# Kernel tuning notes

Measured on AMD Instinct MI355X. Metric: run time of the kernel, lower is better.

Reference implementation:

```python
import jax, jax.numpy as jnp
import numpy as np

N_NODES = 100_000
N_EDGES = 1_600_000
N_GRAPHS = 100
NODES_PER_GRAPH = N_NODES // N_GRAPHS
C_IN = 64
C_EDGE = 16
HIDDEN = 64
N_LAYERS = 3
MLP_HIDDEN = 256
N_CLASSES = 4
ENC = 16  # encoding_size; marker column = ENC-1
BN_EPS = 1e-5


def setup_inputs() -> dict:
    key = jax.random.key(0)
    ks = jax.random.split(key, 12)
    spec_idx = jnp.arange(N_GRAPHS, dtype=jnp.int32) * NODES_PER_GRAPH
    x = jax.random.normal(ks[0], (N_NODES, C_IN), jnp.float32)
    # exactly one specified node per graph: x[:, ENC-1] == 1 only at spec_idx
    x = x.at[:, ENC - 1].set(0.0)
    x = x.at[spec_idx, ENC - 1].set(1.0)
    # edges confined within each graph
    eg = jax.random.randint(ks[1], (N_EDGES,), 0, N_GRAPHS)
    src = eg * NODES_PER_GRAPH + jax.random.randint(ks[2], (N_EDGES,), 0, NODES_PER_GRAPH)
    dst = eg * NODES_PER_GRAPH + jax.random.randint(ks[3], (N_EDGES,), 0, NODES_PER_GRAPH)
    edge_index = jnp.stack([src, dst]).astype(jnp.int32)
    edge_attr = jax.random.normal(ks[4], (N_EDGES, C_EDGE), jnp.float32)
    batch = jnp.repeat(jnp.arange(N_GRAPHS, dtype=jnp.int32), NODES_PER_GRAPH)
    neighbor = jax.random.normal(ks[5], (N_GRAPHS, C_IN), jnp.float32)
    msg_in = 2 * HIDDEN + C_EDGE  # 144 (C_IN == HIDDEN)
    s = 1.0 / np.sqrt(msg_in)
    W = jax.random.normal(ks[6], (N_LAYERS, msg_in, HIDDEN), jnp.float32) * s
    b = jax.random.normal(ks[7], (N_LAYERS, HIDDEN), jnp.float32) * s
    bn_gamma = jnp.ones((N_LAYERS, HIDDEN), jnp.float32)
    bn_beta = jnp.zeros((N_LAYERS, HIDDEN), jnp.float32)
    fc1_in = HIDDEN + C_IN + N_LAYERS * HIDDEN  # 320
    fc1_w = jax.random.normal(ks[8], (fc1_in, MLP_HIDDEN), jnp.float32) / np.sqrt(fc1_in)
    fc1_b = jax.random.normal(ks[9], (MLP_HIDDEN,), jnp.float32) / np.sqrt(fc1_in)
    fc2_w = jax.random.normal(ks[10], (MLP_HIDDEN, N_CLASSES), jnp.float32) / np.sqrt(MLP_HIDDEN)
    fc2_b = jax.random.normal(ks[11], (N_CLASSES,), jnp.float32) / np.sqrt(MLP_HIDDEN)
    return {"x": x, "edge_attr": edge_attr, "neighbor": neighbor, "W": W, "b": b,
            "bn_gamma": bn_gamma, "bn_beta": bn_beta, "fc1_w": fc1_w, "fc1_b": fc1_b,
            "fc2_w": fc2_w, "fc2_b": fc2_b, "edge_index": edge_index, "batch": batch,
            "spec_idx": spec_idx}


def reference(x, edge_attr, neighbor, W, b, bn_gamma, bn_beta,
              fc1_w, fc1_b, fc2_w, fc2_b, edge_index, batch, spec_idx):
    N = x.shape[0]
    loops = jnp.arange(N, dtype=edge_index.dtype)
    src = jnp.concatenate([edge_index[0], loops])   # x_j (source)
    dst = jnp.concatenate([edge_index[1], loops])   # x_i (target / aggregate)
    ea = jnp.concatenate([edge_attr, jnp.ones((N, edge_attr.shape[1]), x.dtype)], axis=0)
    bn_scale = 1.0 / jnp.sqrt(jnp.float32(1.0) + BN_EPS)  # eval BN: mean=0, var=1
    embs = []
    for l in range(W.shape[0]):
        # gather -> linear on concat(x_i, x_j, e) -> scatter-add
        m = jnp.concatenate([x[dst], x[src], ea], axis=1) @ W[l] + b[l]  # [E+N, H]
        agg = jax.ops.segment_sum(m, dst, num_segments=N)                # [N, H]
        h = jax.nn.relu(agg)                       # relu inside MP layer
        h = bn_gamma[l] * h * bn_scale + bn_beta[l]  # BatchNorm1d (eval)
        x = jax.nn.relu(h)                         # relu after BN (dropout=eval no-op)
        embs.append(x[spec_idx])
    B = spec_idx.shape[0]
    pooled = jax.ops.segment_sum(x, batch, num_segments=B)  # global_add_pool [B, H]
    feats = jnp.concatenate([pooled] + embs + [neighbor], axis=1)  # [B, 320]
    h = jax.nn.relu(feats @ fc1_w + fc1_b)
    return h @ fc2_w + fc2_b
```

## Files before the change

kernel.cpp:

```cpp
#include <hip/hip_runtime.h>
#include <hip/hip_bf16.h>

#define NN 100000
#define NE 1600000
#define NG 100
#define NPG 1000
#define CE 16
#define HH 64
#define BN_SCALE 0.99999500003749959f
#define NB 512
#define ECH (NE / NB)
#define NBIN 400
#define NRANGE 12500


typedef __attribute__((ext_vector_type(8))) short bf16x8;
typedef __attribute__((ext_vector_type(4))) float f32x4;
union ABu { bf16x8 f; ushort u[8]; };

__device__ __forceinline__ ushort f2bf_rne(float f) {
  unsigned u = __float_as_uint(f);
  return (ushort)((u + 0x7FFFu + ((u >> 16) & 1u)) >> 16);
}

__global__ __launch_bounds__(256) void k_hist(const int* __restrict__ ei,
                                              int* __restrict__ hist) {
  __shared__ int h[NBIN];
  for (int i = threadIdx.x; i < NBIN; i += 256) h[i] = 0;
  __syncthreads();
  int e0 = blockIdx.x * ECH;
  for (int i = threadIdx.x; i < ECH; i += 256) {
    int d = ei[NE + e0 + i];
    atomicAdd(&h[d / 250], 1);
  }
  __syncthreads();
  for (int i = threadIdx.x; i < NBIN; i += 256) hist[blockIdx.x * NBIN + i] = h[i];
}

__global__ __launch_bounds__(512) void k_scan_a(const int* __restrict__ hist,
                                                int* __restrict__ partial,
                                                int* __restrict__ gtot) {
  __shared__ int sv[512];
  int bin = blockIdx.x, t = threadIdx.x;
  int v = (t < NB) ? hist[t * NBIN + bin] : 0;
  sv[t] = v;
  __syncthreads();
  for (int o = 1; o < 512; o <<= 1) {
    int a = (t >= o) ? sv[t - o] : 0;
    __syncthreads();
    sv[t] += a;
    __syncthreads();
  }
  if (t < NB) partial[t * NBIN + bin] = sv[t] - v;
  if (t == 511) gtot[bin] = sv[511];
}

__global__ __launch_bounds__(512) void k_scan_b(const int* __restrict__ gtot,
                                                int* __restrict__ gbase) {
  __shared__ int sv[512];
  int t = threadIdx.x;
  int v = (t < NBIN) ? gtot[t] : 0;
  sv[t] = v;
  __syncthreads();
  for (int o = 1; o < 512; o <<= 1) {
    int a = (t >= o) ? sv[t - o] : 0;
    __syncthreads();
    sv[t] += a;
    __syncthreads();
  }
  if (t < NBIN) gbase[t] = sv[t] - v;
  if (t == 511) gbase[NBIN] = sv[511];
}

__global__ __launch_bounds__(256) void k_bfill(const int* __restrict__ ei,
                                               const int* __restrict__ partial,
                                               const int* __restrict__ gbase,
                                               unsigned long long* __restrict__ ebuf) {
  __shared__ int cur[NBIN];
  int b = blockIdx.x;
  for (int i = threadIdx.x; i < NBIN; i += 256)
    cur[i] = gbase[i] + partial[b * NBIN + i];
  __syncthreads();
  int e0 = b * ECH;
  for (int i = threadIdx.x; i < ECH; i += 256) {
    int e = e0 + i;
    int d = ei[NE + e], s = ei[e];
    int bin = d / 250;
    int gb = (bin >> 2) * 1000;
    unsigned long long pk = (unsigned long long)(unsigned)e << 32 |
                            (unsigned)((d - gb) << 10) | (unsigned)(s - gb);
    int pos = atomicAdd(&cur[bin], 1);
    ebuf[pos] = pk;
  }
}

__global__ __launch_bounds__(1024) void k_nsort(
    const unsigned long long* __restrict__ ebuf, const int* __restrict__ gbase,
    unsigned* __restrict__ ebuf2, int* __restrict__ rowptr,
    int* __restrict__ cnt) {
  __shared__ int h[250];
  __shared__ int cur[250];
  __shared__ int sv[256];
  int bin = blockIdx.x, t = threadIdx.x;
  int nb = bin * 250, lbase = (bin & 3) * 250;
  int lo = gbase[bin], hi = gbase[bin + 1];
  if (t < 250) h[t] = 0;
  __syncthreads();
  for (int i = lo + t; i < hi; i += 1024) {
    int dl = (int)((ebuf[i] >> 10) & 1023);
    atomicAdd(&h[dl - lbase], 1);
  }
  __syncthreads();
  int v = (t < 250) ? h[t] : 0;
  if (t < 256) sv[t] = v;
  __syncthreads();
  for (int o = 1; o < 256; o <<= 1) {
    int a = (t < 256 && t >= o) ? sv[t - o] : 0;
    __syncthreads();
    if (t < 256) sv[t] += a;
    __syncthreads();
  }
  if (t < 250) {
    int base = lo + sv[t] - v;
    rowptr[nb + t] = base;
    cur[t] = base;
    cnt[nb + t] = v;
  }
  if (bin == NBIN - 1 && t == 0) rowptr[NN] = hi;
  __syncthreads();
  for (int i = lo + t; i < hi; i += 1024) {
    unsigned long long u = ebuf[i];
    int dl = (int)((u >> 10) & 1023);
    unsigned pk = (unsigned)(u >> 32) << 10 | (unsigned)(u & 1023);
    int pos = atomicAdd(&cur[dl - lbase], 1);
    ebuf2[pos] = pk;
  }
}

#define SEB 25000
__global__ __launch_bounds__(256) void k_se3(const unsigned* __restrict__ ebuf2,
                                             const int* __restrict__ rowptr,
                                             const float* __restrict__ ea,
                                             ushort* __restrict__ Se16) {
  int lane = threadIdx.x & 63;
  int slot = lane >> 2;
  int q = lane & 3;
  int orig = blockIdx.x;
  int blk = (orig & 7) * (SEB / 8) + (orig >> 3);
  int n0 = blk * 4 + (threadIdx.x >> 6);
  if (n0 >= NN) return;
  int n = __builtin_amdgcn_readfirstlane(n0);
  int lo = rowptr[n], hi = rowptr[n + 1];
  float aA0 = 0.f, aA1 = 0.f, aA2 = 0.f, aA3 = 0.f;
  float aB0 = 0.f, aB1 = 0.f, aB2 = 0.f, aB3 = 0.f;
  for (int k0 = lo; k0 < hi; k0 += 32) {
    int ka = k0 + slot, kb = k0 + 16 + slot;
    int kca = min(ka, NE - 1), kcb = min(kb, NE - 1);
    unsigned eida = ebuf2[kca] >> 10;
    unsigned eidb = ebuf2[kcb] >> 10;
    float4 va = *(const float4*)(ea + (size_t)eida * CE + q * 4);
    float4 vb = *(const float4*)(ea + (size_t)eidb * CE + q * 4);
    bool oka = ka < hi, okb = kb < hi;
    aA0 += oka ? va.x : 0.f;
    aA1 += oka ? va.y : 0.f;
    aA2 += oka ? va.z : 0.f;
    aA3 += oka ? va.w : 0.f;
    aB0 += okb ? vb.x : 0.f;
    aB1 += okb ? vb.y : 0.f;
    aB2 += okb ? vb.z : 0.f;
    aB3 += okb ? vb.w : 0.f;
  }
  float r0 = aA0 + aB0, r1 = aA1 + aB1, r2 = aA2 + aB2, r3 = aA3 + aB3;
#pragma unroll
  for (int o = 4; o < 64; o <<= 1) {
    r0 += __shfl_xor(r0, o);
    r1 += __shfl_xor(r1, o);
    r2 += __shfl_xor(r2, o);
    r3 += __shfl_xor(r3, o);
  }
  if (lane < 4) {
    unsigned lo32 = (unsigned)f2bf_rne(r0) | ((unsigned)f2bf_rne(r1) << 16);
    unsigned hi32 = (unsigned)f2bf_rne(r2) | ((unsigned)f2bf_rne(r3) << 16);
    *(uint2*)(Se16 + (size_t)n * 16 + lane * 4) = make_uint2(lo32, hi32);
  }
}

__global__ __launch_bounds__(256) void k_cvt(const float* __restrict__ xin,
                                             ushort* __restrict__ xb) {
  int i = blockIdx.x * 256 + threadIdx.x;
  float4 v = ((const float4*)xin)[i];
  ushort4 o;
  o.x = f2bf_rne(v.x); o.y = f2bf_rne(v.y);
  o.z = f2bf_rne(v.z); o.w = f2bf_rne(v.w);
  ((ushort4*)xb)[i] = o;
}

#define GEMM_TILES (NN / 16)
#define GB 512
__global__ __attribute__((amdgpu_waves_per_eu(2, 4))) __launch_bounds__(256)
void k_gemm(const ushort* __restrict__ x, const float* __restrict__ W,
            const float* __restrict__ b, const int* __restrict__ cnt,
            const ushort* __restrict__ Se16, ushort* __restrict__ y,
            ushort* __restrict__ z) {
  int lane = threadIdx.x & 63;
  int g = lane >> 4, r16 = lane & 15;

  ABu Bm[8][2];
  ABu Bs[4];
  float bias4[4];
#pragma unroll
  for (int t = 0; t < 8; ++t) {
    int col = t * 16 + r16;
    const float* wbase = W + (col < 64 ? 0 : 64 * 64);
    int c64 = col & 63;
#pragma unroll
    for (int h = 0; h < 2; ++h)
#pragma unroll
      for (int e = 0; e < 8; ++e) {
        int k = h * 32 + (e < 4 ? 0 : 16) + 4 * g + (e & 3);
        Bm[t][h].u[e] = f2bf_rne(wbase[k * 64 + c64]);
      }
  }
#pragma unroll
  for (int t = 0; t < 4; ++t) {
    int col = t * 16 + r16;
    float ws = 0.f;
#pragma unroll
    for (int m = 0; m < 16; ++m) ws += W[(128 + m) * 64 + col];
#pragma unroll
    for (int e = 0; e < 8; ++e) {
      int k = (e < 4 ? 0 : 16) + 4 * g + (e & 3);
      float v = (k < 16) ? W[(128 + k) * 64 + col] : (k == 16 ? ws : 0.f);
      Bs[t].u[e] = f2bf_rne(v);
    }
    bias4[t] = b[col];
  }

  int wid = (blockIdx.x << 2) + (threadIdx.x >> 6);
  int nw = GB * 4;
  for (int tt = wid; tt < GEMM_TILES; tt += nw) {
    int nb = tt * 16;
    const ushort* xr = x + (size_t)(nb + r16) * 64;
    ABu A0, A1, AS;
    *(ushort4*)&A0.u[0] = *(const ushort4*)(xr + 4 * g);
    *(ushort4*)&A0.u[4] = *(const ushort4*)(xr + 16 + 4 * g);
    *(ushort4*)&A1.u[0] = *(const ushort4*)(xr + 32 + 4 * g);
    *(ushort4*)&A1.u[4] = *(const ushort4*)(xr + 48 + 4 * g);
    const ushort* sr = Se16 + (size_t)(nb + r16) * 16;
    *(ushort4*)&AS.u[0] = *(const ushort4*)(sr + 4 * g);
    AS.u[4] = (g == 0) ? (ushort)0x3F80 : (ushort)0;
    AS.u[5] = 0; AS.u[6] = 0; AS.u[7] = 0;
    float dq[4];
#pragma unroll
    for (int q = 0; q < 4; ++q) dq[q] = (float)(cnt[nb + 4 * g + q] + 1);

    f32x4 accM[8], accS[4];
#pragma unroll
    for (int t = 0; t < 8; ++t) {
      f32x4 zz = {0.f, 0.f, 0.f, 0.f};
      zz = __builtin_amdgcn_mfma_f32_16x16x32_bf16(A0.f, Bm[t][0].f, zz, 0, 0, 0);
      accM[t] = __builtin_amdgcn_mfma_f32_16x16x32_bf16(A1.f, Bm[t][1].f, zz, 0, 0, 0);
    }
#pragma unroll
    for (int t = 0; t < 4; ++t) {
      f32x4 zz = {0.f, 0.f, 0.f, 0.f};
      accS[t] = __builtin_amdgcn_mfma_f32_16x16x32_bf16(AS.f, Bs[t].f, zz, 0, 0, 0);
    }
#pragma unroll
    for (int q = 0; q < 4; ++q) {
      size_t node = (size_t)(nb + 4 * g + q);
      ushort* zp = z + node * 64 + r16;
      ushort* yp = y + node * 64 + r16;
#pragma unroll
      for (int t = 0; t < 4; ++t) {
        float zv = dq[q] * (accM[t][q] + bias4[t]) + accS[t][q];
        zp[t * 16] = f2bf_rne(zv);
        yp[t * 16] = f2bf_rne(accM[4 + t][q]);
      }
    }
  }
}

#define GTB 25000
__global__ __launch_bounds__(256) void k_gath3(
    const __hip_bfloat16* __restrict__ y, const __hip_bfloat16* __restrict__ z,
    const unsigned* __restrict__ ebuf2, const int* __restrict__ rowptr,
    const float* __restrict__ gamma, const float* __restrict__ beta,
    __hip_bfloat16* __restrict__ xn, float* __restrict__ emb) {
  int lane = threadIdx.x & 63;
  int orig = blockIdx.x;
  int blk = (orig & 7) * (GTB / 8) + (orig >> 3);
  int n0 = blk * 4 + (threadIdx.x >> 6);
  if (n0 >= NN) return;
  int n = __builtin_amdgcn_readfirstlane(n0);
  int lo = rowptr[n], hi = rowptr[n + 1];
  int deg = hi - lo;
  int gb = (n / NPG) * NPG;
  const unsigned* cl = ebuf2 + lo;
  const __hip_bfloat16* yg = y + (size_t)gb * HH;
  float acc = __bfloat162float(z[(size_t)n * HH + lane]) +
              __bfloat162float(y[(size_t)n * HH + lane]);
  int k = 0;
  for (; k + 8 <= deg; k += 8) {
    int s0 = cl[k] & 1023, s1 = cl[k + 1] & 1023;
    int s2 = cl[k + 2] & 1023, s3 = cl[k + 3] & 1023;
    int s4 = cl[k + 4] & 1023, s5 = cl[k + 5] & 1023;
    int s6 = cl[k + 6] & 1023, s7 = cl[k + 7] & 1023;
    float v0 = __bfloat162float(yg[(size_t)s0 * HH + lane]);
    float v1 = __bfloat162float(yg[(size_t)s1 * HH + lane]);
    float v2 = __bfloat162float(yg[(size_t)s2 * HH + lane]);
    float v3 = __bfloat162float(yg[(size_t)s3 * HH + lane]);
    float v4 = __bfloat162float(yg[(size_t)s4 * HH + lane]);
    float v5 = __bfloat162float(yg[(size_t)s5 * HH + lane]);
    float v6 = __bfloat162float(yg[(size_t)s6 * HH + lane]);
    float v7 = __bfloat162float(yg[(size_t)s7 * HH + lane]);
    acc += ((v0 + v1) + (v2 + v3)) + ((v4 + v5) + (v6 + v7));
  }
  for (; k < deg; ++k)
    acc += __bfloat162float(yg[(size_t)(cl[k] & 1023) * HH + lane]);
  acc = fmaxf(acc, 0.f);
  acc = gamma[lane] * acc * BN_SCALE + beta[lane];
  acc = fmaxf(acc, 0.f);
  xn[(size_t)n * HH + lane] = __float2bfloat16(acc);
  if (n % NPG == 0) emb[(n / NPG) * HH + lane] = acc;
}

__global__ __launch_bounds__(512) void k_pool(const __hip_bfloat16* __restrict__ xf,
                                              float* __restrict__ partial) {
  __shared__ float pp[8][64];
  int bin = blockIdx.x;
  int lane = threadIdx.x & 63, wv = threadIdx.x >> 6;
  const __hip_bfloat16* base = xf + (size_t)bin * 250 * HH;
  float acc = 0.f;
  int i = wv;
  for (; i + 24 < 250; i += 32) {
    float v0 = __bfloat162float(base[(size_t)i * HH + lane]);
    float v1 = __bfloat162float(base[(size_t)(i + 8) * HH + lane]);
    float v2 = __bfloat162float(base[(size_t)(i + 16) * HH + lane]);
    float v3 = __bfloat162float(base[(size_t)(i + 24) * HH + lane]);
    acc += (v0 + v1) + (v2 + v3);
  }
  for (; i < 250; i += 8) acc += __bfloat162float(base[(size_t)i * HH + lane]);
  pp[wv][lane] = acc;
  __syncthreads();
  if (wv == 0) {
    float s = ((pp[0][lane] + pp[1][lane]) + (pp[2][lane] + pp[3][lane])) +
              ((pp[4][lane] + pp[5][lane]) + (pp[6][lane] + pp[7][lane]));
    partial[bin * 64 + lane] = s;
  }
}

__global__ __launch_bounds__(256) void k_final(
    const float* __restrict__ partial, const float* __restrict__ emb,
    const float* __restrict__ nbr, const float* __restrict__ fc1w,
    const float* __restrict__ fc1b, const float* __restrict__ fc2w,
    const float* __restrict__ fc2b, float* __restrict__ out) {
  __shared__ float feats[320];
  __shared__ float r1[256];
  __shared__ float red[4][4];
  int g = blockIdx.x;
  int t = threadIdx.x;
  if (t < 64) {
    const float* pb = partial + 4 * g * 64;
    feats[t] = (pb[t] + pb[64 + t]) + (pb[128 + t] + pb[192 + t]);
    feats[256 + t] = nbr[(size_t)g * HH + t];
  } else {
    int j = t - 64;
    feats[64 + j] = emb[((size_t)(j >> 6) * NG + g) * HH + (j & 63)];
  }
  __syncthreads();
  float a0 = fc1b[t], a1 = 0.f, a2 = 0.f, a3 = 0.f;
  const float* wp = fc1w + t;
  for (int k = 0; k < 320; k += 8) {
    float w0 = wp[(k + 0) * 256], w1 = wp[(k + 1) * 256];
    float w2 = wp[(k + 2) * 256], w3 = wp[(k + 3) * 256];
    float w4 = wp[(k + 4) * 256], w5 = wp[(k + 5) * 256];
    float w6 = wp[(k + 6) * 256], w7 = wp[(k + 7) * 256];
    a0 = fmaf(feats[k], w0, a0);
    a1 = fmaf(feats[k + 1], w1, a1);
    a2 = fmaf(feats[k + 2], w2, a2);
    a3 = fmaf(feats[k + 3], w3, a3);
    a0 = fmaf(feats[k + 4], w4, a0);
    a1 = fmaf(feats[k + 5], w5, a1);
    a2 = fmaf(feats[k + 6], w6, a2);
    a3 = fmaf(feats[k + 7], w7, a3);
  }
  float rv = fmaxf((a0 + a1) + (a2 + a3), 0.f);
  r1[t] = rv;
  float p0 = rv * fc2w[t * 4 + 0];
  float p1 = rv * fc2w[t * 4 + 1];
  float p2 = rv * fc2w[t * 4 + 2];
  float p3 = rv * fc2w[t * 4 + 3];
#pragma unroll
  for (int o = 1; o < 64; o <<= 1) {
    p0 += __shfl_xor(p0, o);
    p1 += __shfl_xor(p1, o);
    p2 += __shfl_xor(p2, o);
    p3 += __shfl_xor(p3, o);
  }
  if ((t & 63) == 0) {
    int wv = t >> 6;
    red[wv][0] = p0; red[wv][1] = p1; red[wv][2] = p2; red[wv][3] = p3;
  }
  __syncthreads();
  if (t < 4)
    out[g * 4 + t] = fc2b[t] +
                     ((red[0][t] + red[1][t]) + (red[2][t] + red[3][t]));
}

extern "C" void kernel_launch(void* const* d_in, const int* in_sizes, int n_in,
                              void* d_out, int out_size, void* d_ws, size_t ws_size,
                              hipStream_t stream) {
  const float* x     = (const float*)d_in[0];
  const float* eattr = (const float*)d_in[1];
  const float* nbr   = (const float*)d_in[2];
  const float* W     = (const float*)d_in[3];
  const float* b     = (const float*)d_in[4];
  const float* gamma = (const float*)d_in[5];
  const float* beta  = (const float*)d_in[6];
  const float* fc1w  = (const float*)d_in[7];
  const float* fc1b  = (const float*)d_in[8];
  const float* fc2w  = (const float*)d_in[9];
  const float* fc2b  = (const float*)d_in[10];
  const int*   ei    = (const int*)d_in[11];
  float* out = (float*)d_out;
  (void)in_sizes; (void)n_in; (void)out_size; (void)ws_size;

  char* p = (char*)d_ws;
  size_t off = 0;
  auto alloc = [&](size_t bytes) {
    char* q = p + off;
    off += (bytes + 255) & ~(size_t)255;
    return q;
  };
  int* hist    = (int*)alloc((size_t)NB * NBIN * 4);
  int* partial = (int*)alloc((size_t)NB * NBIN * 4);
  int* gtot    = (int*)alloc((size_t)NBIN * 4);
  int* gbase   = (int*)alloc((size_t)(NBIN + 1) * 4);
  unsigned long long* ebuf = (unsigned long long*)alloc((size_t)NE * 8);
  unsigned* ebuf2 = (unsigned*)alloc((size_t)NE * 4);
  int* rowptr  = (int*)alloc((size_t)(NN + 1) * 4);
  ushort* Se16 = (ushort*)alloc((size_t)NN * 16 * 2);
  int*   cnt   = (int*)alloc((size_t)NN * 4);
  ushort* xbf  = (ushort*)alloc((size_t)NN * HH * 2);
  ushort* ybuf = (ushort*)alloc((size_t)NN * HH * 2);
  ushort* zbuf = (ushort*)alloc((size_t)NN * HH * 2);
  ushort* xA   = (ushort*)alloc((size_t)NN * HH * 2);
  ushort* xB   = (ushort*)alloc((size_t)NN * HH * 2);
  float* emb   = (float*)alloc((size_t)3 * NG * HH * 4);
  float* pool  = (float*)alloc((size_t)NBIN * HH * 4);

  k_hist<<<NB, 256, 0, stream>>>(ei, hist);
  k_scan_a<<<NBIN, 512, 0, stream>>>(hist, partial, gtot);
  k_scan_b<<<1, 512, 0, stream>>>(gtot, gbase);
  k_bfill<<<NB, 256, 0, stream>>>(ei, partial, gbase, ebuf);
  k_nsort<<<NBIN, 1024, 0, stream>>>(ebuf, gbase, ebuf2, rowptr, cnt);
  k_se3<<<SEB, 256, 0, stream>>>(ebuf2, rowptr, eattr, Se16);
  k_cvt<<<NN * HH / 4 / 256, 256, 0, stream>>>(x, xbf);

  k_gemm<<<GB, 256, 0, stream>>>(xbf, W, b, cnt, Se16, ybuf, zbuf);
  k_gath3<<<GTB, 256, 0, stream>>>((const __hip_bfloat16*)ybuf,
                                   (const __hip_bfloat16*)zbuf, ebuf2, rowptr,
                                   gamma, beta, (__hip_bfloat16*)xA, emb);
  k_gemm<<<GB, 256, 0, stream>>>(xA, W + 144 * 64, b + 64, cnt, Se16, ybuf, zbuf);
  k_gath3<<<GTB, 256, 0, stream>>>((const __hip_bfloat16*)ybuf,
                                   (const __hip_bfloat16*)zbuf, ebuf2, rowptr,
                                   gamma + 64, beta + 64, (__hip_bfloat16*)xB,
                                   emb + NG * HH);
  k_gemm<<<GB, 256, 0, stream>>>(xB, W + 2 * 144 * 64, b + 128, cnt, Se16, ybuf,
                                 zbuf);
  k_gath3<<<GTB, 256, 0, stream>>>((const __hip_bfloat16*)ybuf,
                                   (const __hip_bfloat16*)zbuf, ebuf2, rowptr,
                                   gamma + 128, beta + 128, (__hip_bfloat16*)xA,
                                   emb + 2 * NG * HH);

  k_pool<<<NBIN, 512, 0, stream>>>((const __hip_bfloat16*)xA, pool);
  k_final<<<NG, 256, 0, stream>>>(pool, emb, nbr, fc1w, fc1b, fc2w, fc2b, out);
}
```

Baseline: 261.3 us.

## Aggregate raw neighbor features before GEMM and fuse BN/ReLU into GEMM epilogue

Reorders each message-passing layer so neighbor features are summed first (gather-then-transform) and the source-side weight is applied to the aggregated sum in the GEMM, instead of transforming every node and then gathering transformed rows. The BN/ReLU epilogue and the spec-node embedding write move into the GEMM, and the first layer reads fp32 x directly, which removes the separate conversion kernel and the y/z intermediate buffers. The gather kernel now processes two nodes per wave with paired loads and clamped, predicated tails. The GEMM gains extra MFMAs and another A operand load per tile. The first-layer gather reads fp32 rows, doubling its traffic for that layer.

```diff
diff --git a/kernel.cpp b/kernel.cpp
--- a/kernel.cpp
+++ b/kernel.cpp
@@ -11,7 +11,6 @@
 #define NB 512
 #define ECH (NE / NB)
 #define NBIN 400
-#define NRANGE 12500
 
 
 typedef __attribute__((ext_vector_type(8))) short bf16x8;
@@ -185,45 +184,93 @@
   }
 }
 
-__global__ __launch_bounds__(256) void k_cvt(const float* __restrict__ xin,
-                                             ushort* __restrict__ xb) {
-  int i = blockIdx.x * 256 + threadIdx.x;
-  float4 v = ((const float4*)xin)[i];
-  ushort4 o;
-  o.x = f2bf_rne(v.x); o.y = f2bf_rne(v.y);
-  o.z = f2bf_rne(v.z); o.w = f2bf_rne(v.w);
-  ((ushort4*)xb)[i] = o;
+#define GXB 12500
+template <typename T>
+__device__ __forceinline__ void ldpair(const T* xg, unsigned srcl, int c,
+                                       float& p0, float& p1) {
+  if constexpr (sizeof(T) == 4) {
+    const float* p = (const float*)xg + (size_t)srcl * HH + 2 * c;
+    p0 = p[0];
+    p1 = p[1];
+  } else {
+    unsigned u = *(const unsigned*)((const ushort*)xg + (size_t)srcl * HH + 2 * c);
+    p0 = __uint_as_float(u << 16);
+    p1 = __uint_as_float(u & 0xffff0000u);
+  }
+}
+
+template <typename T>
+__global__ __launch_bounds__(256) void k_gathx(const T* __restrict__ x,
+                                               const unsigned* __restrict__ ebuf2,
+                                               const int* __restrict__ rowptr,
+                                               ushort* __restrict__ Sx) {
+  int lane = threadIdx.x & 63;
+  int h = lane >> 5, c = lane & 31;
+  int pr = blockIdx.x * 4 + (threadIdx.x >> 6);
+  int n = pr * 2 + h;
+  int lo = rowptr[n], hi = rowptr[n + 1];
+  int deg = hi - lo;
+  int gb = (n / NPG) * NPG;
+  const T* xg = x + (size_t)gb * HH;
+  float a0, a1;
+  ldpair(x, (unsigned)n, c, a0, a1);
+  int kend = hi - 1;
+  for (int k = 0; k < deg; k += 8) {
+    int k0 = lo + k;
+    int c0 = min(k0 + 0, kend), c1 = min(k0 + 1, kend);
+    int c2 = min(k0 + 2, kend), c3 = min(k0 + 3, kend);
+    int c4 = min(k0 + 4, kend), c5 = min(k0 + 5, kend);
+    int c6 = min(k0 + 6, kend), c7 = min(k0 + 7, kend);
+    unsigned s0 = ebuf2[c0] & 1023u, s1 = ebuf2[c1] & 1023u;
+    unsigned s2 = ebuf2[c2] & 1023u, s3 = ebuf2[c3] & 1023u;
+    unsigned s4 = ebuf2[c4] & 1023u, s5 = ebuf2[c5] & 1023u;
+    unsigned s6 = ebuf2[c6] & 1023u, s7 = ebuf2[c7] & 1023u;
+    float v00, v01, v10, v11, v20, v21, v30, v31;
+    float v40, v41, v50, v51, v60, v61, v70, v71;
+    ldpair(xg, s0, c, v00, v01);
+    ldpair(xg, s1, c, v10, v11);
+    ldpair(xg, s2, c, v20, v21);
+    ldpair(xg, s3, c, v30, v31);
+    ldpair(xg, s4, c, v40, v41);
+    ldpair(xg, s5, c, v50, v51);
+    ldpair(xg, s6, c, v60, v61);
+    ldpair(xg, s7, c, v70, v71);
+    bool o0 = k + 0 < deg, o1 = k + 1 < deg, o2 = k + 2 < deg, o3 = k + 3 < deg;
+    bool o4 = k + 4 < deg, o5 = k + 5 < deg, o6 = k + 6 < deg, o7 = k + 7 < deg;
+    a0 += (o0 ? v00 : 0.f) + (o1 ? v10 : 0.f) + (o2 ? v20 : 0.f) + (o3 ? v30 : 0.f);
+    a1 += (o0 ? v01 : 0.f) + (o1 ? v11 : 0.f) + (o2 ? v21 : 0.f) + (o3 ? v31 : 0.f);
+    a0 += (o4 ? v40 : 0.f) + (o5 ? v50 : 0.f) + (o6 ? v60 : 0.f) + (o7 ? v70 : 0.f);
+    a1 += (o4 ? v41 : 0.f) + (o5 ? v51 : 0.f) + (o6 ? v61 : 0.f) + (o7 ? v71 : 0.f);
+  }
+  unsigned w = (unsigned)f2bf_rne(a0) | ((unsigned)f2bf_rne(a1) << 16);
+  *(unsigned*)(Sx + (size_t)n * HH + 2 * c) = w;
 }
 
 #define GEMM_TILES (NN / 16)
 #define GB 512
+template <typename T>
 __global__ __attribute__((amdgpu_waves_per_eu(2, 4))) __launch_bounds__(256)
-void k_gemm(const ushort* __restrict__ x, const float* __restrict__ W,
-            const float* __restrict__ b, const int* __restrict__ cnt,
-            const ushort* __restrict__ Se16, ushort* __restrict__ y,
-            ushort* __restrict__ z) {
+void k_gemm2(const T* __restrict__ x, const ushort* __restrict__ Sx,
+             const float* __restrict__ W, const float* __restrict__ b,
+             const int* __restrict__ cnt, const ushort* __restrict__ Se16,
+             const float* __restrict__ gamma, const float* __restrict__ beta,
+             ushort* __restrict__ xn, float* __restrict__ embL) {
   int lane = threadIdx.x & 63;
   int g = lane >> 4, r16 = lane & 15;
 
-  ABu Bm[8][2];
-  ABu Bs[4];
-  float bias4[4];
-#pragma unroll
-  for (int t = 0; t < 8; ++t) {
-    int col = t * 16 + r16;
-    const float* wbase = W + (col < 64 ? 0 : 64 * 64);
-    int c64 = col & 63;
-#pragma unroll
-    for (int h = 0; h < 2; ++h)
-#pragma unroll
-      for (int e = 0; e < 8; ++e) {
-        int k = h * 32 + (e < 4 ? 0 : 16) + 4 * g + (e & 3);
-        Bm[t][h].u[e] = f2bf_rne(wbase[k * 64 + c64]);
-      }
-  }
+  ABu Bi[4][2], Bj[4][2], Bs[4];
+  float bias4[4], gam4[4], bet4[4];
 #pragma unroll
   for (int t = 0; t < 4; ++t) {
     int col = t * 16 + r16;
+#pragma unroll
+    for (int hh = 0; hh < 2; ++hh)
+#pragma unroll
+      for (int e = 0; e < 8; ++e) {
+        int k = hh * 32 + (e < 4 ? 0 : 16) + 4 * g + (e & 3);
+        Bi[t][hh].u[e] = f2bf_rne(W[k * 64 + col]);
+        Bj[t][hh].u[e] = f2bf_rne(W[(64 + k) * 64 + col]);
+      }
     float ws = 0.f;
 #pragma unroll
     for (int m = 0; m < 16; ++m) ws += W[(128 + m) * 64 + col];
@@ -234,18 +281,41 @@
       Bs[t].u[e] = f2bf_rne(v);
     }
     bias4[t] = b[col];
+    gam4[t] = gamma[col] * BN_SCALE;
+    bet4[t] = beta[col];
   }
 
   int wid = (blockIdx.x << 2) + (threadIdx.x >> 6);
   int nw = GB * 4;
   for (int tt = wid; tt < GEMM_TILES; tt += nw) {
     int nb = tt * 16;
-    const ushort* xr = x + (size_t)(nb + r16) * 64;
-    ABu A0, A1, AS;
-    *(ushort4*)&A0.u[0] = *(const ushort4*)(xr + 4 * g);
-    *(ushort4*)&A0.u[4] = *(const ushort4*)(xr + 16 + 4 * g);
-    *(ushort4*)&A1.u[0] = *(const ushort4*)(xr + 32 + 4 * g);
-    *(ushort4*)&A1.u[4] = *(const ushort4*)(xr + 48 + 4 * g);
+    ABu A0, A1, X0, X1, AS;
+    if constexpr (sizeof(T) == 4) {
+      const float* xr = (const float*)x + (size_t)(nb + r16) * HH;
+      float4 f0 = *(const float4*)(xr + 4 * g);
+      float4 f1 = *(const float4*)(xr + 16 + 4 * g);
+      float4 f2 = *(const float4*)(xr + 32 + 4 * g);
+      float4 f3 = *(const float4*)(xr + 48 + 4 * g);
+      A0.u[0] = f2bf_rne(f0.x); A0.u[1] = f2bf_rne(f0.y);
+      A0.u[2] = f2bf_rne(f0.z); A0.u[3] = f2bf_rne(f0.w);
+      A0.u[4] = f2bf_rne(f1.x); A0.u[5] = f2bf_rne(f1.y);
+      A0.u[6] = f2bf_rne(f1.z); A0.u[7] = f2bf_rne(f1.w);
+      A1.u[0] = f2bf_rne(f2.x); A1.u[1] = f2bf_rne(f2.y);
+      A1.u[2] = f2bf_rne(f2.z); A1.u[3] = f2bf_rne(f2.w);
+      A1.u[4] = f2bf_rne(f3.x); A1.u[5] = f2bf_rne(f3.y);
+      A1.u[6] = f2bf_rne(f3.z); A1.u[7] = f2bf_rne(f3.w);
+    } else {
+      const ushort* xr = (const ushort*)x + (size_t)(nb + r16) * HH;
+      *(ushort4*)&A0.u[0] = *(const ushort4*)(xr + 4 * g);
+      *(ushort4*)&A0.u[4] = *(const ushort4*)(xr + 16 + 4 * g);
+      *(ushort4*)&A1.u[0] = *(const ushort4*)(xr + 32 + 4 * g);
+      *(ushort4*)&A1.u[4] = *(const ushort4*)(xr + 48 + 4 * g);
+    }
+    const ushort* sxr = Sx + (size_t)(nb + r16) * HH;
+    *(ushort4*)&X0.u[0] = *(const ushort4*)(sxr + 4 * g);
+    *(ushort4*)&X0.u[4] = *(const ushort4*)(sxr + 16 + 4 * g);
+    *(ushort4*)&X1.u[0] = *(const ushort4*)(sxr + 32 + 4 * g);
+    *(ushort4*)&X1.u[4] = *(const ushort4*)(sxr + 48 + 4 * g);
     const ushort* sr = Se16 + (size_t)(nb + r16) * 16;
     *(ushort4*)&AS.u[0] = *(const ushort4*)(sr + 4 * g);
     AS.u[4] = (g == 0) ? (ushort)0x3F80 : (ushort)0;
@@ -254,75 +324,33 @@
 #pragma unroll
     for (int q = 0; q < 4; ++q) dq[q] = (float)(cnt[nb + 4 * g + q] + 1);
 
-    f32x4 accM[8], accS[4];
-#pragma unroll
-    for (int t = 0; t < 8; ++t) {
-      f32x4 zz = {0.f, 0.f, 0.f, 0.f};
-      zz = __builtin_amdgcn_mfma_f32_16x16x32_bf16(A0.f, Bm[t][0].f, zz, 0, 0, 0);
-      accM[t] = __builtin_amdgcn_mfma_f32_16x16x32_bf16(A1.f, Bm[t][1].f, zz, 0, 0, 0);
-    }
+    f32x4 accI[4], accR[4];
 #pragma unroll
     for (int t = 0; t < 4; ++t) {
       f32x4 zz = {0.f, 0.f, 0.f, 0.f};
-      accS[t] = __builtin_amdgcn_mfma_f32_16x16x32_bf16(AS.f, Bs[t].f, zz, 0, 0, 0);
+      zz = __builtin_amdgcn_mfma_f32_16x16x32_bf16(A0.f, Bi[t][0].f, zz, 0, 0, 0);
+      accI[t] = __builtin_amdgcn_mfma_f32_16x16x32_bf16(A1.f, Bi[t][1].f, zz, 0, 0, 0);
+      f32x4 rr = {0.f, 0.f, 0.f, 0.f};
+      rr = __builtin_amdgcn_mfma_f32_16x16x32_bf16(X0.f, Bj[t][0].f, rr, 0, 0, 0);
+      rr = __builtin_amdgcn_mfma_f32_16x16x32_bf16(X1.f, Bj[t][1].f, rr, 0, 0, 0);
+      accR[t] = __builtin_amdgcn_mfma_f32_16x16x32_bf16(AS.f, Bs[t].f, rr, 0, 0, 0);
     }
 #pragma unroll
     for (int q = 0; q < 4; ++q) {
-      size_t node = (size_t)(nb + 4 * g + q);
-      ushort* zp = z + node * 64 + r16;
-      ushort* yp = y + node * 64 + r16;
+      int node = nb + 4 * g + q;
+      ushort* xp = xn + (size_t)node * 64 + r16;
+      bool spec = (node % NPG) == 0;
 #pragma unroll
       for (int t = 0; t < 4; ++t) {
-        float zv = dq[q] * (accM[t][q] + bias4[t]) + accS[t][q];
-        zp[t * 16] = f2bf_rne(zv);
-        yp[t * 16] = f2bf_rne(accM[4 + t][q]);
+        float zv = dq[q] * (accI[t][q] + bias4[t]) + accR[t][q];
+        zv = fmaxf(zv, 0.f);
+        zv = gam4[t] * zv + bet4[t];
+        zv = fmaxf(zv, 0.f);
+        xp[t * 16] = f2bf_rne(zv);
+        if (spec) embL[(node / NPG) * HH + t * 16 + r16] = zv;
       }
     }
   }
-}
-
-#define GTB 25000
-__global__ __launch_bounds__(256) void k_gath3(
-    const __hip_bfloat16* __restrict__ y, const __hip_bfloat16* __restrict__ z,
-    const unsigned* __restrict__ ebuf2, const int* __restrict__ rowptr,
-    const float* __restrict__ gamma, const float* __restrict__ beta,
-    __hip_bfloat16* __restrict__ xn, float* __restrict__ emb) {
-  int lane = threadIdx.x & 63;
-  int orig = blockIdx.x;
-  int blk = (orig & 7) * (GTB / 8) + (orig >> 3);
-  int n0 = blk * 4 + (threadIdx.x >> 6);
-  if (n0 >= NN) return;
-  int n = __builtin_amdgcn_readfirstlane(n0);
-  int lo = rowptr[n], hi = rowptr[n + 1];
-  int deg = hi - lo;
-  int gb = (n / NPG) * NPG;
-  const unsigned* cl = ebuf2 + lo;
-  const __hip_bfloat16* yg = y + (size_t)gb * HH;
-  float acc = __bfloat162float(z[(size_t)n * HH + lane]) +
-              __bfloat162float(y[(size_t)n * HH + lane]);
-  int k = 0;
-  for (; k + 8 <= deg; k += 8) {
-    int s0 = cl[k] & 1023, s1 = cl[k + 1] & 1023;
-    int s2 = cl[k + 2] & 1023, s3 = cl[k + 3] & 1023;
-    int s4 = cl[k + 4] & 1023, s5 = cl[k + 5] & 1023;
-    int s6 = cl[k + 6] & 1023, s7 = cl[k + 7] & 1023;
-    float v0 = __bfloat162float(yg[(size_t)s0 * HH + lane]);
-    float v1 = __bfloat162float(yg[(size_t)s1 * HH + lane]);
-    float v2 = __bfloat162float(yg[(size_t)s2 * HH + lane]);
-    float v3 = __bfloat162float(yg[(size_t)s3 * HH + lane]);
-    float v4 = __bfloat162float(yg[(size_t)s4 * HH + lane]);
-    float v5 = __bfloat162float(yg[(size_t)s5 * HH + lane]);
-    float v6 = __bfloat162float(yg[(size_t)s6 * HH + lane]);
-    float v7 = __bfloat162float(yg[(size_t)s7 * HH + lane]);
-    acc += ((v0 + v1) + (v2 + v3)) + ((v4 + v5) + (v6 + v7));
-  }
-  for (; k < deg; ++k)
-    acc += __bfloat162float(yg[(size_t)(cl[k] & 1023) * HH + lane]);
-  acc = fmaxf(acc, 0.f);
-  acc = gamma[lane] * acc * BN_SCALE + beta[lane];
-  acc = fmaxf(acc, 0.f);
-  xn[(size_t)n * HH + lane] = __float2bfloat16(acc);
-  if (n % NPG == 0) emb[(n / NPG) * HH + lane] = acc;
 }
 
 __global__ __launch_bounds__(512) void k_pool(const __hip_bfloat16* __restrict__ xf,
@@ -442,9 +470,7 @@
   int* rowptr  = (int*)alloc((size_t)(NN + 1) * 4);
   ushort* Se16 = (ushort*)alloc((size_t)NN * 16 * 2);
   int*   cnt   = (int*)alloc((size_t)NN * 4);
-  ushort* xbf  = (ushort*)alloc((size_t)NN * HH * 2);
-  ushort* ybuf = (ushort*)alloc((size_t)NN * HH * 2);
-  ushort* zbuf = (ushort*)alloc((size_t)NN * HH * 2);
+  ushort* Sx   = (ushort*)alloc((size_t)NN * HH * 2);
   ushort* xA   = (ushort*)alloc((size_t)NN * HH * 2);
   ushort* xB   = (ushort*)alloc((size_t)NN * HH * 2);
   float* emb   = (float*)alloc((size_t)3 * NG * HH * 4);
@@ -456,23 +482,17 @@
   k_bfill<<<NB, 256, 0, stream>>>(ei, partial, gbase, ebuf);
   k_nsort<<<NBIN, 1024, 0, stream>>>(ebuf, gbase, ebuf2, rowptr, cnt);
   k_se3<<<SEB, 256, 0, stream>>>(ebuf2, rowptr, eattr, Se16);
-  k_cvt<<<NN * HH / 4 / 256, 256, 0, stream>>>(x, xbf);
-
-  k_gemm<<<GB, 256, 0, stream>>>(xbf, W, b, cnt, Se16, ybuf, zbuf);
-  k_gath3<<<GTB, 256, 0, stream>>>((const __hip_bfloat16*)ybuf,
-                                   (const __hip_bfloat16*)zbuf, ebuf2, rowptr,
-                                   gamma, beta, (__hip_bfloat16*)xA, emb);
-  k_gemm<<<GB, 256, 0, stream>>>(xA, W + 144 * 64, b + 64, cnt, Se16, ybuf, zbuf);
-  k_gath3<<<GTB, 256, 0, stream>>>((const __hip_bfloat16*)ybuf,
-                                   (const __hip_bfloat16*)zbuf, ebuf2, rowptr,
-                                   gamma + 64, beta + 64, (__hip_bfloat16*)xB,
-                                   emb + NG * HH);
-  k_gemm<<<GB, 256, 0, stream>>>(xB, W + 2 * 144 * 64, b + 128, cnt, Se16, ybuf,
-                                 zbuf);
-  k_gath3<<<GTB, 256, 0, stream>>>((const __hip_bfloat16*)ybuf,
-                                   (const __hip_bfloat16*)zbuf, ebuf2, rowptr,
-                                   gamma + 128, beta + 128, (__hip_bfloat16*)xA,
-                                   emb + 2 * NG * HH);
+
+  k_gathx<float><<<GXB, 256, 0, stream>>>(x, ebuf2, rowptr, Sx);
+  k_gemm2<float><<<GB, 256, 0, stream>>>(x, Sx, W, b, cnt, Se16, gamma, beta,
+                                         xA, emb);
+  k_gathx<ushort><<<GXB, 256, 0, stream>>>(xA, ebuf2, rowptr, Sx);
+  k_gemm2<ushort><<<GB, 256, 0, stream>>>(xA, Sx, W + 144 * 64, b + 64, cnt, Se16,
+                                          gamma + 64, beta + 64, xB, emb + NG * HH);
+  k_gathx<ushort><<<GXB, 256, 0, stream>>>(xB, ebuf2, rowptr, Sx);
+  k_gemm2<ushort><<<GB, 256, 0, stream>>>(xB, Sx, W + 2 * 144 * 64, b + 128, cnt,
+                                          Se16, gamma + 128, beta + 128, xA,
+                                          emb + 2 * NG * HH);
 
   k_pool<<<NBIN, 512, 0, stream>>>((const __hip_bfloat16*)xA, pool);
   k_final<<<NG, 256, 0, stream>>>(pool, emb, nbr, fc1w, fc1b, fc2w, fc2b, out);
```

After: 271.1 us. 1.04x slower.
